# Performance work log

Hardware: AMD Instinct MI355X
Metric: run time of the kernel (lower is better)

Reference implementation:

```python
import jax, jax.numpy as jnp
import numpy as np

B, T, N_ITEMS, S = 32, 100, 100000, 1


def setup_inputs() -> dict:
    key = jax.random.key(0)
    k1, k2, k3, k4 = jax.random.split(key, 4)
    output = jax.random.normal(k1, (B, T, N_ITEMS), dtype=jnp.float32)
    labels = jax.random.randint(k2, (B, T), 0, N_ITEMS, dtype=jnp.int64)
    # valid sequence lengths, at least 1 to avoid empty-sequence division
    x_lens = jax.random.randint(k3, (B,), 1, T + 1, dtype=jnp.int64)
    # precomputed negative samples (replaces host-side rejection sampling)
    neg_ids = jax.random.randint(k4, (B, T, S), 0, N_ITEMS, dtype=jnp.int64)
    uids = jnp.arange(B, dtype=jnp.int64)
    return {"output": output, "labels": labels, "x_lens": x_lens,
            "neg_ids": neg_ids, "uids": uids}


def reference(output, labels, x_lens, neg_ids, uids):
    # output: [B, T, N], labels: [B, T], x_lens: [B], neg_ids: [B, T, S]
    pos = jnp.take_along_axis(output, labels[..., None], axis=2)   # [B, T, 1]
    neg = jnp.take_along_axis(output, neg_ids, axis=2)             # [B, T, S]
    logsig = jax.nn.log_sigmoid(pos - neg)                         # [B, T, S]
    per_t = jnp.sum(logsig, axis=-1)                               # [B, T] (sum over samples dim)
    mask = (jnp.arange(T)[None, :] < x_lens[:, None]).astype(per_t.dtype)  # [B, T]
    # per-user: mean over valid timesteps of summed logsigmoid, negated
    per_user = jnp.sum(per_t * mask, axis=1) / x_lens.astype(per_t.dtype)  # [B]
    return -jnp.mean(per_user)
```

## Files before the change

### kernel.cpp

```cpp
#include <hip/hip_runtime.h>


#define B_ 32
#define T_ 100
#define N_ 100000
#define S_ 1
#define NTHREADS 1024

__global__ __launch_bounds__(NTHREADS) void bpr_loss_kernel(
    const float* __restrict__ output,
    const int*   __restrict__ labels,
    const int*   __restrict__ x_lens,
    const int*   __restrict__ neg_ids,
    float*       __restrict__ out)
{
    const int tid = threadIdx.x;
    float acc = 0.f;

    for (int i = tid; i < B_ * T_; i += NTHREADS) {
        const int b = i / T_;
        const int t = i - b * T_;
        const int xl = x_lens[b];
        if (t < xl) {
            const int lab = labels[i];
            const float* row = output + (size_t)i * N_;
            const float pos = row[lab];
            float s = 0.f;
#pragma unroll
            for (int sj = 0; sj < S_; ++sj) {
                const int nid = neg_ids[i * S_ + sj];
                const float neg = row[nid];
                const float x = pos - neg;
                s += fminf(x, 0.f) - log1pf(expf(-fabsf(x)));
            }
            acc += s / (float)xl;
        }
    }

    for (int off = 32; off > 0; off >>= 1)
        acc += __shfl_down(acc, off, 64);

    __shared__ float wsum[NTHREADS / 64];
    const int wid  = tid >> 6;
    const int lane = tid & 63;
    if (lane == 0) wsum[wid] = acc;
    __syncthreads();

    if (wid == 0) {
        float v = (lane < (NTHREADS / 64)) ? wsum[lane] : 0.f;
        for (int off = 8; off > 0; off >>= 1)
            v += __shfl_down(v, off, 64);
        if (lane == 0) out[0] = -v / (float)B_;
    }
}

extern "C" void kernel_launch(void* const* d_in, const int* in_sizes, int n_in,
                              void* d_out, int out_size, void* d_ws, size_t ws_size,
                              hipStream_t stream) {
    const float* output  = (const float*)d_in[0];
    const int*   labels  = (const int*)  d_in[1];
    const int*   x_lens  = (const int*)  d_in[2];
    const int*   neg_ids = (const int*)  d_in[3];
    float* out = (float*)d_out;

    bpr_loss_kernel<<<1, NTHREADS, 0, stream>>>(output, labels, x_lens, neg_ids, out);
}
```

Measured before the change: 10.23 us.

## Split loss into multi-block partial-sum kernel plus final reduction kernel

Replaces the single 1024-thread block with 50 one-wavefront blocks, each handling one (b,t) item per thread and writing a per-block partial sum to workspace. A second single-wavefront kernel reduces the partials. The aim is to spread the dependent gather loads (index fetch, then the row element) across many CUs and drop the serial per-thread loop. In exchange it adds a second kernel launch and a round trip through global memory. It also now performs the gathers for masked timesteps instead of skipping them.

New measurement: 11.31 us. +10.5%, slower.

```diff
diff --git a/kernel.cpp b/kernel.cpp
--- a/kernel.cpp
+++ b/kernel.cpp
@@ -1,57 +1,50 @@
 #include <hip/hip_runtime.h>
 
 
-#define B_ 32
-#define T_ 100
-#define N_ 100000
-#define S_ 1
-#define NTHREADS 1024
+#define B_     32
+#define T_     100
+#define N_     100000
+#define NITEMS (B_ * T_)
+#define NBLK   (NITEMS / 64)
 
-__global__ __launch_bounds__(NTHREADS) void bpr_loss_kernel(
+__global__ __launch_bounds__(64) void bpr_partial_kernel(
     const float* __restrict__ output,
     const int*   __restrict__ labels,
     const int*   __restrict__ x_lens,
     const int*   __restrict__ neg_ids,
+    float*       __restrict__ partials)
+{
+    const int i = blockIdx.x * 64 + threadIdx.x;
+
+    const int b   = i / T_;
+    const int t   = i - b * T_;
+    const int lab = labels[i];
+    const int nid = neg_ids[i];
+    const int xl  = x_lens[b];
+
+    const float* row = output + (size_t)i * N_;
+    const float pos = row[lab];
+    const float neg = row[nid];
+
+    const float x = pos - neg;
+    float v = (t < xl ? 1.0f / (float)xl : 0.0f)
+              * (fminf(x, 0.f) - log1pf(expf(-fabsf(x))));
+
+    for (int off = 32; off > 0; off >>= 1)
+        v += __shfl_down(v, off, 64);
+
+    if (threadIdx.x == 0) partials[blockIdx.x] = v;
+}
+
+__global__ __launch_bounds__(64) void bpr_final_kernel(
+    const float* __restrict__ partials,
     float*       __restrict__ out)
 {
     const int tid = threadIdx.x;
-    float acc = 0.f;
-
-    for (int i = tid; i < B_ * T_; i += NTHREADS) {
-        const int b = i / T_;
-        const int t = i - b * T_;
-        const int xl = x_lens[b];
-        if (t < xl) {
-            const int lab = labels[i];
-            const float* row = output + (size_t)i * N_;
-            const float pos = row[lab];
-            float s = 0.f;
-#pragma unroll
-            for (int sj = 0; sj < S_; ++sj) {
-                const int nid = neg_ids[i * S_ + sj];
-                const float neg = row[nid];
-                const float x = pos - neg;
-                s += fminf(x, 0.f) - log1pf(expf(-fabsf(x)));
-            }
-            acc += s / (float)xl;
-        }
-    }
-
+    float v = (tid < NBLK) ? partials[tid] : 0.f;
     for (int off = 32; off > 0; off >>= 1)
-        acc += __shfl_down(acc, off, 64);
-
-    __shared__ float wsum[NTHREADS / 64];
-    const int wid  = tid >> 6;
-    const int lane = tid & 63;
-    if (lane == 0) wsum[wid] = acc;
-    __syncthreads();
-
-    if (wid == 0) {
-        float v = (lane < (NTHREADS / 64)) ? wsum[lane] : 0.f;
-        for (int off = 8; off > 0; off >>= 1)
-            v += __shfl_down(v, off, 64);
-        if (lane == 0) out[0] = -v / (float)B_;
-    }
+        v += __shfl_down(v, off, 64);
+    if (tid == 0) out[0] = -v / (float)B_;
 }
 
 extern "C" void kernel_launch(void* const* d_in, const int* in_sizes, int n_in,
@@ -61,7 +54,9 @@
     const int*   labels  = (const int*)  d_in[1];
     const int*   x_lens  = (const int*)  d_in[2];
     const int*   neg_ids = (const int*)  d_in[3];
-    float* out = (float*)d_out;
+    float* out      = (float*)d_out;
+    float* partials = (float*)d_ws;
 
-    bpr_loss_kernel<<<1, NTHREADS, 0, stream>>>(output, labels, x_lens, neg_ids, out);
+    bpr_partial_kernel<<<NBLK, 64, 0, stream>>>(output, labels, x_lens, neg_ids, partials);
+    bpr_final_kernel<<<1, 64, 0, stream>>>(partials, out);
 }
```
